# Performance work log

Measured on AMD Instinct MI355X. Metric: run time of the kernel, lower is better.

The kernel has to match this reference:

```python
import jax, jax.numpy as jnp
from jax import lax
import numpy as np

D = 1024   # d_model
N = 64     # d_state
P = 64     # headdim
H = 16     # nheads = d_inner // headdim (d_inner = d_model)
E = 8      # n_experts
R = 8      # LoRA rank
OM = 32    # omega_dim
MEMD = 384 # memory vector dim
KC = 4     # d_conv
Bz, Lz = 2, 1024


def setup_inputs() -> dict:
    key = jax.random.key(0)
    it = iter(jax.random.split(key, 48))
    def nrm(shape, s=0.02):
        return jax.random.normal(next(it), shape, jnp.float32) * s
    return dict(
        x=jax.random.normal(next(it), (Bz, Lz, D), jnp.float32),
        wkv_state=nrm((Bz, N, N), 0.1),
        x_prev=jax.random.normal(next(it), (Bz, 1, D), jnp.float32),
        memory_vec=jax.random.normal(next(it), (Bz, MEMD), jnp.float32),
        rag_state=nrm((Bz, N, N), 0.1),
        ssd_state=nrm((Bz, H, P, N), 0.1),
        conv_state=nrm((Bz, D, KC), 0.1),
        norm_scale=jnp.ones((D,), jnp.float32), norm_bias=jnp.zeros((D,), jnp.float32),
        W_in=nrm((2 * D, D)), conv_w=nrm((D, KC), 0.1), conv_b=jnp.zeros((D,), jnp.float32),
        W_dt=nrm((H, D)), dt_bias=jnp.full((H,), -2.0, jnp.float32),
        A_log=jnp.log(jnp.linspace(0.5, 8.0, H)).astype(jnp.float32),
        W_B=nrm((N, D)), W_C=nrm((N, D)), W_ssd_out=nrm((D, D)),
        W_r=nrm((N, D)), W_k=nrm((N, D)), W_v=nrm((N, D)), W_w=nrm((N, D)),
        W_rwkv_out=nrm((D, N)),
        W_skew=nrm((OM, OM), 0.1), W_om_in=nrm((OM, D)), W_om_out=nrm((D, OM)),
        W_router=nrm((E, D)), lora_A=nrm((E, D, R)), lora_B=nrm((E, R, D)),
        W_nov=nrm((1, 2 * D)), b_nov=jnp.zeros((1,), jnp.float32),
        W_ragq=nrm((N, D)), W_rago=nrm((D, N)),
        W_mq=nrm((MEMD, D)), W_mp=nrm((D, MEMD)),
        W_mg=nrm((1, D + MEMD)), b_mg=jnp.zeros((1,), jnp.float32),
    )


def _layernorm(x, s, b):
    m = x.mean(-1, keepdims=True)
    v = ((x - m) ** 2).mean(-1, keepdims=True)
    return (x - m) * lax.rsqrt(v + 1e-5) * s + b


def _forward(x, wkv_state, x_prev, memory_vec, rag_state, ssd_state, conv_state,
             norm_scale, norm_bias, W_in, conv_w, conv_b, W_dt, dt_bias, A_log,
             W_B, W_C, W_ssd_out, W_r, W_k, W_v, W_w, W_rwkv_out,
             W_skew, W_om_in, W_om_out, W_router, lora_A, lora_B, W_nov, b_nov,
             W_ragq, W_rago, W_mq, W_mp, W_mg, b_mg):
    Bb, Ll, _ = x.shape
    residual = x
    xn = _layernorm(x, norm_scale, norm_bias)
    # ---- TarsCoreBlock: Mamba-2 SSD scan + RWKV-7 wkv scan + gated fusion ----
    zu = xn @ W_in.T
    z, u = zu[..., :D], zu[..., D:]
    # depthwise causal conv1d with rolling conv_state [B, D, KC]
    u_cat = jnp.concatenate([conv_state.transpose(0, 2, 1), u], axis=1)  # [B, KC+L, D]
    acc = conv_b
    for k in range(KC):
        acc = acc + u_cat[:, k:k + Ll, :] * conv_w[:, k]
    uc = jax.nn.silu(acc)
    conv_new = u_cat[:, Ll:, :].transpose(0, 2, 1)
    dt = jax.nn.softplus(xn @ W_dt.T + dt_bias)   # [B,L,H]
    A = -jnp.exp(A_log)                            # [H], negative decay rates
    Bm = xn @ W_B.T                                # [B,L,N]
    Cm = xn @ W_C.T                                # [B,L,N]
    uh = uc.reshape(Bb, Ll, H, P)
    def ssd_step(h, inp):
        dt_t, u_t, b_t, c_t = inp                  # [B,H],[B,H,P],[B,N],[B,N]
        h = h * jnp.exp(dt_t * A)[..., None, None] + (dt_t[..., None, None] * u_t[..., None]) * b_t[:, None, None, :]
        return h, jnp.einsum('bhpn,bn->bhp', h, c_t)
    ssd_new, ys = lax.scan(ssd_step, ssd_state,
                           (dt.transpose(1, 0, 2), uh.transpose(1, 0, 2, 3),
                            Bm.transpose(1, 0, 2), Cm.transpose(1, 0, 2)))
    y_ssd = ys.transpose(1, 0, 2, 3).reshape(Bb, Ll, D) @ W_ssd_out.T
    # RWKV-7 style wkv recurrence with time-shift mixing
    x_shift = jnp.concatenate([x_prev, xn[:, :-1]], axis=1)
    mix = 0.5 * (xn + x_shift)
    r, kk, v = mix @ W_r.T, mix @ W_k.T, mix @ W_v.T
    w = jnp.exp(-jnp.exp(mix @ W_w.T))             # per-channel decay in (0,1)
    def rwkv_step(S, inp):
        r_t, k_t, v_t, w_t = inp
        S = S * w_t[:, :, None] + v_t[:, :, None] * k_t[:, None, :]
        return S, jnp.einsum('bij,bj->bi', S, r_t)
    wkv_new, yr = lax.scan(rwkv_step, wkv_state,
                           (r.transpose(1, 0, 2), kk.transpose(1, 0, 2),
                            v.transpose(1, 0, 2), w.transpose(1, 0, 2)))
    y_rwkv = yr.transpose(1, 0, 2) @ W_rwkv_out.T
    core_out = jax.nn.silu(z) * y_ssd + y_rwkv     # WuNeng fusion
    x1 = residual + core_out
    x_prev_new = xn[:, -1:, :]
    # ---- RAG injection from compressed rag_state ----
    q = x1.mean(1) @ W_ragq.T                      # [B,N]
    info = jnp.einsum('bij,bj->bi', rag_state, q)
    x1 = x1 + 0.1 * (info @ W_rago.T)[:, None, :]
    # ---- Omega-SSM: Cayley SO(n) rotation in omega subspace ----
    Ask = 0.5 * (W_skew - W_skew.T)
    I = jnp.eye(OM, dtype=x.dtype)
    Qc = jnp.linalg.solve(I - Ask, I + Ask)        # orthogonal via Cayley map
    x1 = x1 + ((x1 @ W_om_in.T) @ Qc.T) @ W_om_out.T
    # ---- MoLE: sparse top-2 low-rank (LoRA) experts ----
    probs = jax.nn.softmax(x1 @ W_router.T, axis=-1)  # [B,L,E]
    _, topi = lax.top_k(probs, 2)
    mask = jax.nn.one_hot(topi, E, dtype=x.dtype).sum(-2)
    gate = probs * mask
    gate = gate / (gate.sum(-1, keepdims=True) + 1e-9)
    down = jnp.einsum('bld,edr->bler', x1, lora_A)    # [B,L,E,R]
    x2 = x1 + jnp.einsum('bler,erd->bld', down * gate[..., None], lora_B)
    aux = E * jnp.sum(probs.mean((0, 1)) * mask.mean((0, 1)))
    # ---- NoveltyGate blended residual ----
    h_old, h_new = residual.mean(1), x2.mean(1)
    novelty = jax.nn.sigmoid(jnp.concatenate([h_old, h_new], -1) @ W_nov.T + b_nov)[:, 0]
    n = novelty[:, None, None]
    x3 = n * x2 + (1.0 - n) * residual
    # ---- Cosine-gated memory fusion ----
    h_post = x3.mean(1)
    hq = h_post @ W_mq.T
    sim = (hq * memory_vec).sum(-1) / (jnp.linalg.norm(hq, axis=-1) * jnp.linalg.norm(memory_vec, axis=-1) + 1e-8)
    gm = jax.nn.sigmoid(jnp.concatenate([h_post, memory_vec], -1) @ W_mg.T + b_mg)[:, 0]
    x4 = x3 + (sim * gm)[:, None, None] * (memory_vec @ W_mp.T)[:, None, :]
    return x4, wkv_new, x_prev_new, ssd_new, conv_new, aux


def reference(x, wkv_state, x_prev, memory_vec, rag_state, ssd_state, conv_state,
              norm_scale, norm_bias, W_in, conv_w, conv_b, W_dt, dt_bias, A_log,
              W_B, W_C, W_ssd_out, W_r, W_k, W_v, W_w, W_rwkv_out,
              W_skew, W_om_in, W_om_out, W_router, lora_A, lora_B, W_nov, b_nov,
              W_ragq, W_rago, W_mq, W_mp, W_mg, b_mg):
    return _forward(x, wkv_state, x_prev, memory_vec, rag_state, ssd_state, conv_state,
                    norm_scale, norm_bias, W_in, conv_w, conv_b, W_dt, dt_bias, A_log,
                    W_B, W_C, W_ssd_out, W_r, W_k, W_v, W_w, W_rwkv_out,
                    W_skew, W_om_in, W_om_out, W_router, lora_A, lora_B, W_nov, b_nov,
                    W_ragq, W_rago, W_mq, W_mp, W_mg, b_mg)
```

## Files before the change

kernel.cpp:

```cpp
#include <hip/hip_runtime.h>
#include <hip/hip_bf16.h>

#define DD    1024
#define NN    64
#define HH    16
#define EE    8
#define OMM   32
#define MEMDD 384
#define BB    2
#define LL    1024
#define TT    2048

#define OFF_X4    0
#define OFF_WKV   2097152
#define OFF_XPREV 2105344
#define OFF_SSD   2107392
#define OFF_CONV  2238464
#define OFF_AUX   2246656

typedef unsigned short u16;
typedef __attribute__((ext_vector_type(8))) short short8;
typedef __attribute__((ext_vector_type(4))) float f32x4;

__device__ __forceinline__ float us2f(u16 u){ return __uint_as_float(((unsigned)u)<<16); }
// ... 217 lines not shown
        for (int n=0;n<4;++n) acc[m][n] = (f32x4){0.f,0.f,0.f,0.f};
    for (int k0=0; k0<K; k0+=64){
        #pragma unroll
        for (int i=0;i<2;++i){
            int row = wid*16 + i*8 + lr;
            gl_lds16(Ag + (size_t)row*K + k0 + lc8, &Asm[(wid*16 + i*8)*64]);
        }
        #pragma unroll
        for (int i=0;i<4;++i){
            int row = wid*32 + i*8 + lr;
            gl_lds16(Wg + (size_t)row*K + k0 + lc8, &Bsm[(wid*32 + i*8)*64]);
        }
        __syncthreads();
        #pragma unroll
        for (int ks=0; ks<2; ++ks){
            short8 af[2], bf[4];
            #pragma unroll
            for (int m=0;m<2;++m)
                af[m] = *(const short8*)&Asm[(wr*32 + m*16 + l15)*64 + ks*32 + quad*8];
            #pragma unroll
            for (int n=0;n<4;++n)
                bf[n] = *(const short8*)&Bsm[(wc*64 + n*16 + l15)*64 + ks*32 + quad*8];
            #pragma unroll
            for (int m=0;m<2;++m)
                #pragma unroll
                for (int n=0;n<4;++n)
                    acc[m][n] = __builtin_amdgcn_mfma_f32_16x16x32_bf16(af[m], bf[n], acc[m][n], 0,0,0);
        }
        __syncthreads();
    }
    int ns1 = N - Nsplit;
    #pragma unroll
    for (int m=0;m<2;++m){
        #pragma unroll
        for (int n=0;n<4;++n){
            int col = bn + wc*64 + n*16 + l15;
            #pragma unroll
            for (int i=0;i<4;++i){
                int row = bm + wr*32 + m*16 + quad*4 + i;
                float v = acc[m][n][i];
                if (col < Nsplit){
                    size_t id = (size_t)row*Nsplit + col;
                    if (c0bf) ((u16*)C0)[id] = f2us(v);
                    else C0[id] = (addto ? C0[id] : 0.f) + v;
                } else {
                    size_t id = (size_t)row*ns1 + (col - Nsplit);
                    C1[id] = v;
                }
            }
        }
    }
}

__global__ __launch_bounds__(256)
void gemm_big_k(const u16* __restrict__ A, const u16* __restrict__ W,
                float* __restrict__ C0, float* __restrict__ C1,
                int N, int K, int Nsplit, int addto){
    __shared__ u16 Asm[64*64];
    __shared__ u16 Bsm[128*64];
    gemm_body(Asm, Bsm, A, W, C0, C1, N, K, Nsplit, addto, 0, blockIdx.x, blockIdx.y);
}

__global__ __launch_bounds__(256)
void gemm_big2_k(const u16* __restrict__ A, const u16* __restrict__ W,
                 float* __restrict__ C0, float* __restrict__ C1,
                 int N, int K, int Nsplit){
    __shared__ u16 Asm[128*64];
    __shared__ u16 Bsm[128*64];
    int tid = threadIdx.x;
    int wid = tid >> 6, lane = tid & 63;
    int l15 = lane & 15, quad = lane >> 4;
    int wr = wid >> 1, wc = wid & 1;
    int bm = blockIdx.x*128, bn = blockIdx.y*128;
    int lr = lane >> 3;
    int lc8 = (lane & 7)*8;
    const u16* Ag = A + (size_t)bm*K;
    const u16* Wg = W + (size_t)bn*K;
    f32x4 acc[4][4];
    #pragma unroll
    for (int m=0;m<4;++m)
        #pragma unroll
        for (int n=0;n<4;++n) acc[m][n] = (f32x4){0.f,0.f,0.f,0.f};
    for (int k0=0; k0<K; k0+=64){
        #pragma unroll
        for (int i=0;i<4;++i){
            int row = wid*32 + i*8 + lr;
            gl_lds16(Ag + (size_t)row*K + k0 + lc8, &Asm[(wid*32 + i*8)*64]);
        }
        #pragma unroll
        for (int i=0;i<4;++i){
            int row = wid*32 + i*8 + lr;
            gl_lds16(Wg + (size_t)row*K + k0 + lc8, &Bsm[(wid*32 + i*8)*64]);
        }
        __syncthreads();
        #pragma unroll
        for (int ks=0; ks<2; ++ks){
            short8 af[4], bf[4];
            #pragma unroll
            for (int m=0;m<4;++m)
                af[m] = *(const short8*)&Asm[(wr*64 + m*16 + l15)*64 + ks*32 + quad*8];
            #pragma unroll
            for (int n=0;n<4;++n)
                bf[n] = *(const short8*)&Bsm[(wc*64 + n*16 + l15)*64 + ks*32 + quad*8];
            #pragma unroll
            for (int m=0;m<4;++m)
                #pragma unroll
                for (int n=0;n<4;++n)
                    acc[m][n] = __builtin_amdgcn_mfma_f32_16x16x32_bf16(af[m], bf[n], acc[m][n], 0,0,0);
        }
        __syncthreads();
    }
    int ns1 = N - Nsplit;
    #pragma unroll
    for (int m=0;m<4;++m){
        #pragma unroll
        for (int n=0;n<4;++n){
            int col = bn + wc*64 + n*16 + l15;
            #pragma unroll
            for (int i=0;i<4;++i){
                int row = bm + wr*64 + m*16 + quad*4 + i;
                float v = acc[m][n][i];
                if (col < Nsplit){
                    C0[(size_t)row*Nsplit + col] = v;
                } else {
                    C1[(size_t)row*ns1 + (col - Nsplit)] = v;
                }
            }
        }
    }
}

__global__ __launch_bounds__(256)
void proj_dual_k(const u16* __restrict__ xnbf, const u16* __restrict__ wcatxn,
                 float* __restrict__ pcat2_as_f, float* __restrict__ dtraw,
                 const u16* __restrict__ mixbf, const u16* __restrict__ wcatmix,
                 float* __restrict__ rkvw){
    __shared__ u16 Asm[64*64];
    __shared__ u16 Bsm[128*64];
    if (blockIdx.y < 2)
        gemm_body(Asm, Bsm, xnbf, wcatxn, pcat2_as_f, dtraw, 256, 1024, 128, 0, 1, blockIdx.x, blockIdx.y);
    else
        gemm_body(Asm, Bsm, mixbf, wcatmix, rkvw, dtraw, 256, 1024, 256, 0, 0, blockIdx.x, blockIdx.y-2);
}

__global__ __launch_bounds__(256)
void out_dual_k(const u16* __restrict__ ysbf, const u16* __restrict__ wbfss, float* __restrict__ s1,
                const u16* __restrict__ ybf, const u16* __restrict__ wbfrw, float* __restrict__ s2){
    __shared__ u16 Asm[64*64];
    __shared__ u16 Bsm[128*64];
    if (blockIdx.y < 8)
        gemm_body(Asm, Bsm, ysbf, wbfss, s1, (float*)nullptr, 1024, 1024, 1024, 0, 0, blockIdx.x, blockIdx.y);
    else
        gemm_body(Asm, Bsm, ybf, wbfrw, s2, (float*)nullptr, 1024, 64, 1024, 0, 0, blockIdx.x, blockIdx.y-8);
}

__global__ __launch_bounds__(256)
void cmx_k(const float* __restrict__ u, const float* __restrict__ xn,
           const void* __restrict__ cs, const void* __restrict__ cw, const void* __restrict__ cb,
           const void* __restrict__ xprev,
           float* __restrict__ uc, u16* __restrict__ mixbf, void* __restrict__ out,
           const int* modep){
    const int m = *modep;
    int idx = blockIdx.x*256 + threadIdx.x;
    int t = idx >> 10, d = idx & 1023;
    int b = t >> 10, l = t & 1023;
    float acc = LD(cb, d, m);
    #pragma unroll
    for (int k=0;k<4;++k){
        int i = l + k;
        float xv = (i < 4) ? LD(cs, ((size_t)(b*DD + d))*4 + i, m)
                           : u[(size_t)(t + k - 4)*DD + d];
        acc += xv * LD(cw, d*4 + k, m);
    }
    uc[idx] = acc * sigf(acc);
    float xc = xn[idx];
    float xp = (l == 0) ? LD(xprev, (size_t)b*DD + d, m) : xn[idx - DD];
    mixbf[idx] = f2us(0.5f*(xc + xp));
    if (l >= LL-4)
        ST(out, OFF_CONV + (size_t)b*DD*4 + d*4 + (l - (LL-4)), u[idx], m);
}

#define LDSS 72
__global__ __launch_bounds__(256)
void ssdA_k(const u16* __restrict__ pcat2, const float* __restrict__ dtraw,
            const float* __restrict__ uc,
            const void* __restrict__ A_log, const void* __restrict__ dt_bias,
            float* __restrict__ ys, float* __restrict__ Scb, float* __restrict__ cumsb,
            const int* modep){
    __shared__ u16 Bs[64*LDSS];
    __shared__ u16 Cs[64*LDSS];
    __shared__ u16 BTw[64*LDSS];
    __shared__ u16 XTs[64*LDSS];
    __shared__ float cums[64];
    __shared__ float dts_raw[64];
    const int m = *modep;
    int tid = threadIdx.x;
    int wid = tid >> 6, lane = tid & 63;
    int blk = blockIdx.x;
    int b = blk >> 8, h = (blk >> 4) & 15, c = blk & 15;
    int l16 = lane & 15, quad = lane >> 4;
    int r = tid >> 2;
    int cb4 = (tid & 3) * 16;
    float Ah = -expf(LD(A_log, h, m));
    int t0 = c*64;
    const u16* Pg = pcat2 + (size_t)(b*LL + t0)*128;
    #pragma unroll
// ... 43 lines not shown
    __syncthreads();
    f32x4 gacc[4];
    #pragma unroll
    for (int nt=0;nt<4;++nt) gacc[nt]=(f32x4){0.f,0.f,0.f,0.f};
    #pragma unroll
    for (int ks=0; ks<64; ks+=32){
        short8 af = *(const short8*)&Cs[(wid*16 + l16)*LDSS + ks + quad*8];
        #pragma unroll
        for (int nt=0;nt<4;++nt){
            short8 bf = *(const short8*)&Bs[(nt*16 + l16)*LDSS + ks + quad*8];
            gacc[nt] = __builtin_amdgcn_mfma_f32_16x16x32_bf16(af, bf, gacc[nt], 0,0,0);
        }
    }
    __syncthreads();
    #pragma unroll
    for (int nt=0;nt<4;++nt){
        int s_loc = nt*16 + l16;
        #pragma unroll
        for (int i=0;i<4;++i){
            int t_loc = wid*16 + quad*4 + i;
            float gv = (s_loc <= t_loc) ? gacc[nt][i]*expf(cums[t_loc]-cums[s_loc]) : 0.f;
            Bs[t_loc*LDSS + s_loc] = f2us(gv);
        }
    }
    __syncthreads();
    f32x4 acc2[4], acc4[4];
    #pragma unroll
    for (int nt=0;nt<4;++nt){ acc2[nt]=(f32x4){0.f,0.f,0.f,0.f}; acc4[nt]=(f32x4){0.f,0.f,0.f,0.f}; }
    #pragma unroll
    for (int ks=0; ks<64; ks+=32){
        short8 sf = *(const short8*)&Bs[(wid*16 + l16)*LDSS + ks + quad*8];
        short8 xf = *(const short8*)&XTs[(wid*16 + l16)*LDSS + ks + quad*8];
        #pragma unroll
        for (int nt=0;nt<4;++nt){
            short8 xo = *(const short8*)&XTs[(nt*16 + l16)*LDSS + ks + quad*8];
            acc2[nt] = __builtin_amdgcn_mfma_f32_16x16x32_bf16(sf, xo, acc2[nt], 0,0,0);
            short8 bo = *(const short8*)&BTw[(nt*16 + l16)*LDSS + ks + quad*8];
            acc4[nt] = __builtin_amdgcn_mfma_f32_16x16x32_bf16(xf, bo, acc4[nt], 0,0,0);
        }
    }
    #pragma unroll
    for (int nt=0;nt<4;++nt){
        int col = nt*16 + l16;
        #pragma unroll
        for (int i=0;i<4;++i){
            int row = wid*16 + quad*4 + i;
            ys[(size_t)(b*LL + t0 + row)*DD + h*64 + col] = acc2[nt][i];
            Scb[(size_t)blk*4096 + row*64 + col] = acc4[nt][i];
        }
    }
}

#define FS 68
__global__ __launch_bounds__(256)
void rwkvA_k(const float* __restrict__ rkvw,
             float* __restrict__ yr, float* __restrict__ Slb, float* __restrict__ Wcumb){
    __shared__ float wch[64*FS], vch[64*FS], kch[64*FS], rch[64*FS];
    __shared__ float Wc[64*FS];
    __shared__ float part[4*8*64];
    int tid = threadIdx.x;
    int wid = tid >> 6, lane = tid & 63;
    int blk = blockIdx.x;
    int b = blk >> 4, c = blk & 15;
    int t0 = c*64;
    int r = tid >> 2, c4 = (tid & 3)*16;
    const float* base = rkvw + (size_t)(b*LL + t0)*256;
    #pragma unroll
    for (int i=0;i<4;++i){
        int cc = c4 + i*4;
        *(float4*)&rch[r*FS+cc] = *(const float4*)(base + (size_t)r*256 + cc);
        *(float4*)&kch[r*FS+cc] = *(const float4*)(base + (size_t)r*256 + 64 + cc);
        *(float4*)&vch[r*FS+cc] = *(const float4*)(base + (size_t)r*256 + 128 + cc);
        float4 wv = *(const float4*)(base + (size_t)r*256 + 192 + cc);
        wch[r*FS+cc+0] = expf(-expf(wv.x));
        wch[r*FS+cc+1] = expf(-expf(wv.y));
        wch[r*FS+cc+2] = expf(-expf(wv.z));
        wch[r*FS+cc+3] = expf(-expf(wv.w));
    }
    __syncthreads();
    if (wid == 0){
        float cum = 1.f;
        for (int t=0;t<64;++t){ cum *= wch[t*FS+lane]; Wc[t*FS+lane] = cum; }
    }
    __syncthreads();
    #pragma unroll
    for (int q=0;q<16;++q){
        int idx = q*256 + tid;
        int t = idx >> 6, i = idx & 63;
        Wcumb[(size_t)blk*4096 + idx] = Wc[t*FS + i];
    }
    float S[16];
    #pragma unroll
    for (int jj=0;jj<16;++jj) S[jj]=0.f;
    int jb = wid*16;
    for (int t8=0; t8<8; ++t8){
        float ya[8];
        #pragma unroll
        for (int u=0;u<8;++u){
            int t = t8*8+u;
            float wv = wch[t*FS+lane];
            float vv = vch[t*FS+lane];
            float yy0=0.f, yy1=0.f, yy2=0.f, yy3=0.f;
            #pragma unroll
            for (int jj=0;jj<16;jj+=4){
                float k0v = kch[t*FS + jb + jj+0], r0v = rch[t*FS + jb + jj+0];
                float k1v = kch[t*FS + jb + jj+1], r1v = rch[t*FS + jb + jj+1];
                float k2v = kch[t*FS + jb + jj+2], r2v = rch[t*FS + jb + jj+2];
                float k3v = kch[t*FS + jb + jj+3], r3v = rch[t*FS + jb + jj+3];
                S[jj+0] = S[jj+0]*wv + vv*k0v; yy0 += S[jj+0]*r0v;
                S[jj+1] = S[jj+1]*wv + vv*k1v; yy1 += S[jj+1]*r1v;
                S[jj+2] = S[jj+2]*wv + vv*k2v; yy2 += S[jj+2]*r2v;
                S[jj+3] = S[jj+3]*wv + vv*k3v; yy3 += S[jj+3]*r3v;
            }
            ya[u] = (yy0+yy1)+(yy2+yy3);
        }
        #pragma unroll
        for (int u=0;u<8;++u) part[wid*512 + u*64 + lane] = ya[u];
        __syncthreads();
        #pragma unroll
        for (int it=0; it<2; ++it){
            int e = it*256 + tid;
            int u = e >> 6, i = e & 63;
            float y = part[0*512 + u*64 + i] + part[1*512 + u*64 + i]
                    + part[2*512 + u*64 + i] + part[3*512 + u*64 + i];
            yr[(size_t)(b*LL + t0 + t8*8 + u)*NN + i] = y;
        }
        __syncthreads();
    }
    #pragma unroll
    for (int jj=0;jj<16;++jj)
        Slb[(size_t)blk*4096 + (size_t)lane*64 + jb + jj] = S[jj];
}

__global__ __launch_bounds__(256)
void sb_k(const void* __restrict__ ssd_state, const float* __restrict__ Scb,
          const float* __restrict__ cumsb, u16* __restrict__ hinb,
          const void* __restrict__ wkv_state, const float* __restrict__ Slb,
          const float* __restrict__ Wcumb, u16* __restrict__ hinr,
          void* __restrict__ out, const int* modep){
    const int m = *modep;
    int tid = threadIdx.x;
    if (blockIdx.x < 32){
        int bh = blockIdx.x;
        float h[16];
        #pragma unroll
        for (int i=0;i<16;++i)
            h[i] = LD(ssd_state, (size_t)bh*4096 + i*256 + tid, m);
        for (int c=0; c<16; ++c){
            int blk = bh*16 + c;
            float efull = expf(cumsb[(size_t)blk*64 + 63]);
            #pragma unroll
            for (int i=0;i<16;++i){
                hinb[(size_t)blk*4096 + i*256 + tid] = f2us(h[i]);
                h[i] = efull*h[i] + Scb[(size_t)blk*4096 + i*256 + tid];
            }
        }
        #pragma unroll
        for (int i=0;i<16;++i)
            ST(out, OFF_SSD + (size_t)bh*4096 + i*256 + tid, h[i], m);
    } else {
        int b = blockIdx.x - 32;
        float S[16];
        #pragma unroll
        for (int q=0;q<16;++q)
            S[q] = LD(wkv_state, (size_t)b*4096 + q*256 + tid, m);
        for (int c=0;c<16;++c){
            int blk = b*16+c;
            #pragma unroll
            for (int q=0;q<16;++q){
                int idx = q*256+tid;
                int i = idx >> 6;
                hinr[(size_t)blk*4096 + idx] = f2us(S[q]);
                float P = Wcumb[(size_t)blk*4096 + 63*64 + i];
                S[q] = S[q]*P + Slb[(size_t)blk*4096 + idx];
            }
        }
        #pragma unroll
        for (int q=0;q<16;++q)
            ST(out, OFF_WKV + (size_t)b*4096 + q*256 + tid, S[q], m);
    }
}

__global__ __launch_bounds__(256)
// ... 45 lines not shown
                float e = expf(cumsb[(size_t)blk*64 + row]);
                size_t id = (size_t)(b*LL + t0 + row)*DD + h*64 + col;
                ysbf[id] = f2us(ys[id] + e*acc[nt][i]);
            }
        }
    } else {
        int blk = blockIdx.x - 512;
        int b = blk >> 4, c = blk & 15;
        int t0 = c*64;
        const float* Rg = rkvw + (size_t)(b*LL + t0)*256;
        #pragma unroll
        for (int i=0;i<4;++i){
            int cc = cb4 + i*4;
            float4 g = *(const float4*)(Rg + (size_t)r*256 + cc);
            u16* d2 = &T0[r*LDSS + cc];
            d2[0]=f2us(g.x); d2[1]=f2us(g.y); d2[2]=f2us(g.z); d2[3]=f2us(g.w);
            ushort4 hv = *(const ushort4*)(hinr + (size_t)blk*4096 + r*64 + cc);
            u16* hd = &T1[r*LDSS + cc];
            hd[0]=hv.x; hd[1]=hv.y; hd[2]=hv.z; hd[3]=hv.w;
        }
        __syncthreads();
        f32x4 acc[4];
        #pragma unroll
        for (int nt=0;nt<4;++nt) acc[nt]=(f32x4){0.f,0.f,0.f,0.f};
        #pragma unroll
        for (int ks=0; ks<64; ks+=32){
            short8 af = *(const short8*)&T0[(wid*16 + l16)*LDSS + ks + quad*8];
            #pragma unroll
            for (int nt=0;nt<4;++nt){
                short8 hf = *(const short8*)&T1[(nt*16 + l16)*LDSS + ks + quad*8];
                acc[nt] = __builtin_amdgcn_mfma_f32_16x16x32_bf16(af, hf, acc[nt], 0,0,0);
            }
        }
        #pragma unroll
        for (int nt=0;nt<4;++nt){
            int col = nt*16 + l16;
            #pragma unroll
            for (int i=0;i<4;++i){
                int row = wid*16 + quad*4 + i;
                float Wt = Wcumb[(size_t)blk*4096 + row*64 + col];
                size_t id = (size_t)(b*LL + t0 + row)*NN + col;
                ybf[id] = f2us(yr[id] + Wt*acc[nt][i]);
            }
        }
    }
}

__global__ __launch_bounds__(256)
void fuse_mean_k(const float* __restrict__ z, const float* __restrict__ s1,
                 const float* __restrict__ s2, const void* __restrict__ xin,
                 float* __restrict__ x1, float* __restrict__ mean1, const int* modep){
    const int m = *modep;
    int bid = blockIdx.x;
    int lc = bid & 15, dc = (bid >> 4) & 3, b = bid >> 6;
    int d = dc*256 + threadIdx.x;
    float sum = 0.f;
    int l0 = lc*64;
    for (int l=l0; l<l0+64; ++l){
        size_t idx = (size_t)(b*LL + l)*DD + d;
        float zl = z[idx];
        float v = LD(xin, idx, m) + zl*sigf(zl)*s1[idx] + s2[idx];
        x1[idx] = v;
        sum += v;
    }
    atomicAdd(&mean1[b*DD + d], sum*(1.f/LL));
}

__global__ __launch_bounds__(256)
void ragA_k(const float* __restrict__ mean1, const void* __restrict__ W_ragq,
            float* __restrict__ qb, const int* modep){
    const int m = *modep;
    int bx = blockIdx.x;
    int b = bx >> 4;
    int tid = threadIdx.x, wid = tid >> 6, lane = tid & 63;
    int row = (bx & 15)*4 + wid;
    float s = 0.f;
    size_t wo = (size_t)row*DD;
    #pragma unroll
    for (int it=0; it<16; ++it)
        s += LD(W_ragq, wo + it*64 + lane, m) * mean1[(b<<10) + it*64 + lane];
    s = wave_sum64(s);
    if (lane == 0) qb[b*64 + row] = s;
}

__global__ __launch_bounds__(256)
void ragB_k(const float* __restrict__ qb, const void* __restrict__ rag_state,
            float* __restrict__ infob, const int* modep){
    const int m = *modep;
    int bx = blockIdx.x;
    int b = bx >> 4;
    int tid = threadIdx.x, wid = tid >> 6, lane = tid & 63;
    int row = (bx & 15)*4 + wid;
    float s = LD(rag_state, (size_t)(b*64+row)*64 + lane, m) * qb[b*64 + lane];
    s = wave_sum64(s);
    if (lane == 0) infob[b*64 + row] = s;
}

__global__ __launch_bounds__(256)
void ragC_k(const float* __restrict__ infob, const void* __restrict__ W_rago,
            float* __restrict__ ragd, const int* modep){
    const int m = *modep;
    int bx = blockIdx.x;
    int b = bx >> 6;
    int tid = threadIdx.x, wid = tid >> 6, lane = tid & 63;
    int r0 = (bx & 63)*16 + wid*4;
    float iv = infob[b*64 + lane];
    #pragma unroll
    for (int rr=0; rr<4; ++rr){
        int d = r0 + rr;
        float s = iv * LD(W_rago, (size_t)d*64 + lane, m);
        s = wave_sum64(s);
        if (lane == 0) ragd[(b<<10) + d] = 0.1f*s;
    }
}

__global__ __launch_bounds__(256)
void addrag_k(float* __restrict__ x1, const float* __restrict__ ragd, u16* __restrict__ xbf){
    int i4 = (blockIdx.x*256 + threadIdx.x)*4;
    int b = i4 >> 20, d = i4 & 1023;
    #pragma unroll
    for (int j=0;j<4;++j){
        float v = x1[i4+j] + ragd[(b<<10) + d + j];
        x1[i4+j] = v;
        xbf[i4+j] = f2us(v);
    }
}

__global__ __launch_bounds__(256)
void moe_k(const float* __restrict__ x1, const void* __restrict__ W_router,
           const void* __restrict__ lora_A, const void* __restrict__ lora_B,
           float* __restrict__ x2, float* __restrict__ probs8, int* __restrict__ eidx,
           const int* modep){
    const int m = *modep;
    int t = blockIdx.x, tid = threadIdx.x;
    int wid = tid >> 6, lane = tid & 63;
    __shared__ float xs[1024];
    __shared__ float red[32];
    __shared__ float logits[8];
    __shared__ float downs[16];
    __shared__ float gsh[2];
    __shared__ int esh[2];
    #pragma unroll
    for (int i=0;i<4;i++) xs[i*256+tid] = x1[(size_t)t*DD + i*256+tid];
    __syncthreads();
    {
        float p0=0.f, p1=0.f;
        size_t w0o = (size_t)(2*wid)*DD, w1o = (size_t)(2*wid+1)*DD;
        #pragma unroll
        for (int it=0; it<16; ++it){
            float xv = xs[it*64 + lane];
            p0 += xv * LD(W_router, w0o + it*64 + lane, m);
            p1 += xv * LD(W_router, w1o + it*64 + lane, m);
        }
        p0 = wave_sum64(p0); p1 = wave_sum64(p1);
        if (lane == 0){ logits[2*wid] = p0; logits[2*wid+1] = p1; }
    }
    __syncthreads();
    if (tid == 0){
        float mx = logits[0];
// ... 3 lines not shown
        for (int e2=0;e2<8;++e2) pe[e2] /= sum;
        int e0=0; for (int e2=1;e2<8;++e2) if (pe[e2]>pe[e0]) e0=e2;
        int e1=(e0==0)?1:0; for (int e2=0;e2<8;++e2) if (e2!=e0 && pe[e2]>pe[e1]) e1=e2;
        float gs = pe[e0]+pe[e1]+1e-9f;
        gsh[0]=pe[e0]/gs; gsh[1]=pe[e1]/gs; esh[0]=e0; esh[1]=e1;
        #pragma unroll
        for (int e2=0;e2<8;++e2) probs8[(size_t)t*8 + e2] = pe[e2];
        eidx[t*2+0]=e0; eidx[t*2+1]=e1;
    }
    __syncthreads();
    {
        int ei = wid & 1, half = wid >> 1;
        int e2 = esh[ei];
        int dsub = lane >> 3;
        size_t ao = (size_t)e2*8192 + (size_t)half*4096;
        float acc = 0.f;
        #pragma unroll
        for (int c=0; c<64; ++c){
            float xv = xs[half*512 + c*8 + dsub];
            acc += xv * LD(lora_A, ao + c*64 + lane, m);
        }
        acc += __shfl_xor(acc, 8);
        acc += __shfl_xor(acc, 16);
        acc += __shfl_xor(acc, 32);
        if (lane < 8) red[wid*8 + lane] = acc;
    }
    __syncthreads();
    if (tid < 16){
        int ei = tid >> 3, r = tid & 7;
        downs[ei*8 + r] = red[ei*8 + r] + red[(ei+2)*8 + r];
    }
    __syncthreads();
    {
        int e0=esh[0], e1=esh[1]; float g0=gsh[0], g1=gsh[1];
        #pragma unroll
        for (int i=0;i<4;i++){
            int d = i*256+tid;
            float acc=0.f;
            size_t b0 = (size_t)e0*8192 + d;
            size_t b1 = (size_t)e1*8192 + d;
            #pragma unroll
            for (int r=0;r<8;++r) acc += g0*downs[r]*LD(lora_B, b0 + (size_t)r*1024, m)
                                       + g1*downs[8+r]*LD(lora_B, b1 + (size_t)r*1024, m);
            x2[(size_t)t*DD + d] = xs[d] + acc;
        }
    }
}

__global__ __launch_bounds__(256)
void colmean2_k(const float* __restrict__ x2, const void* __restrict__ xin,
                float* __restrict__ hnew, float* __restrict__ hold, const int* modep){
    const int m = *modep;
    int bid = blockIdx.x;
    int lc = bid & 15, dc = (bid >> 4) & 3, b = bid >> 6;
    int d = dc*256 + threadIdx.x;
    float s = 0.f;
    int l0 = lc*64;
    if (blockIdx.y == 0){
        for (int l=l0; l<l0+64; ++l) s += x2[(size_t)(b*LL + l)*DD + d];
        atomicAdd(&hnew[b*DD + d], s*(1.f/LL));
    } else {
        for (int l=l0; l<l0+64; ++l) s += LD(xin, (size_t)(b*LL + l)*DD + d, m);
        atomicAdd(&hold[b*DD + d], s*(1.f/LL));
    }
}

__global__ __launch_bounds__(256)
void hq2_k(const float* __restrict__ hold, const float* __restrict__ hnew,
           const void* __restrict__ W_nov, const void* __restrict__ b_nov,
           const void* __restrict__ W_mq, float* __restrict__ hqb, const int* modep){
    const int m = *modep;
    int b = blockIdx.x, tid = threadIdx.x;
    int wid = tid >> 6, lane = tid & 63;
    int r0 = blockIdx.y*16;
    __shared__ float hs[1024];
    __shared__ float red[256];
    float p=0.f;
    #pragma unroll
    for (int i=0;i<4;i++){ int d=i*256+tid;
        p += hold[b*DD+d]*LD(W_nov,d,m) + hnew[b*DD+d]*LD(W_nov,DD+d,m); }
    float n = sigf(block_sum256(p, red) + LD(b_nov,0,m));
    #pragma unroll
    for (int i=0;i<4;i++){ int d=i*256+tid;
        hs[d] = n*hnew[b*DD+d] + (1.f-n)*hold[b*DD+d]; }
    __syncthreads();
    #pragma unroll
    for (int rr=0; rr<4; ++rr){
        int row = r0 + wid*4 + rr;
        float s = 0.f;
        size_t wo = (size_t)row*DD;
        #pragma unroll
        for (int it=0; it<16; ++it) s += LD(W_mq, wo + it*64 + lane, m) * hs[it*64 + lane];
        s = wave_sum64(s);
        if (lane == 0) hqb[b*MEMDD + row] = s;
    }
}

__global__ __launch_bounds__(256)
void gate2_k(const float* __restrict__ hold, const float* __restrict__ hnew,
             const void* __restrict__ W_nov, const void* __restrict__ b_nov,
             const float* __restrict__ hqb, const void* __restrict__ memv,
             const void* __restrict__ W_mg, const void* __restrict__ b_mg,
             const float* __restrict__ probs8, const int* __restrict__ eidx,
             float* __restrict__ scal, void* __restrict__ out, const int* modep){
    const int m = *modep;
    int b = blockIdx.x, tid = threadIdx.x;
    int wid = tid >> 6, lane = tid & 63;
    __shared__ float red[256];
    __shared__ float rps[4][8];
    __shared__ float rcs[4][8];
    float p=0.f;
    #pragma unroll
    for (int i=0;i<4;i++){ int d=i*256+tid;
        p += hold[b*DD+d]*LD(W_nov,d,m) + hnew[b*DD+d]*LD(W_nov,DD+d,m); }
    float n = sigf(block_sum256(p, red) + LD(b_nov,0,m));
// ... 72 lines not shown
    cb rag_state = d_in[4];
    cb ssd_state = d_in[5];
    cb conv_state= d_in[6];
    cb nscale    = d_in[7];
    cb nbias     = d_in[8];
    cb W_in      = d_in[9];
    cb conv_w    = d_in[10];
    cb conv_b    = d_in[11];
    cb W_dt      = d_in[12];
    cb dt_bias   = d_in[13];
    cb A_log     = d_in[14];
    cb W_B       = d_in[15];
    cb W_C       = d_in[16];
    cb W_ssd_out = d_in[17];
    cb W_r       = d_in[18];
    cb W_k       = d_in[19];
    cb W_v       = d_in[20];
    cb W_w       = d_in[21];
    cb W_rwkv_out= d_in[22];
    cb W_skew    = d_in[23];
    cb W_om_in   = d_in[24];
    cb W_om_out  = d_in[25];
    cb W_router  = d_in[26];
    cb lora_A    = d_in[27];
    cb lora_B    = d_in[28];
    cb W_nov     = d_in[29];
    cb b_nov     = d_in[30];
    cb W_ragq    = d_in[31];
    cb W_rago    = d_in[32];
    cb W_mq      = d_in[33];
    cb W_mp      = d_in[34];
    cb W_mg      = d_in[35];
    cb b_mg      = d_in[36];

    float* ws = (float*)d_ws;
    size_t o = 0;
    float* xn_x1   = ws + o; o += (size_t)TT*DD;
    float* z_x2    = ws + o; o += (size_t)TT*DD;
    float* u_ys    = ws + o; o += (size_t)TT*DD;
    float* ucb     = ws + o; o += (size_t)TT*DD;
    float* s2b     = ws + o; o += (size_t)TT*DD;
    float* dtraw   = ws + o; o += (size_t)TT*128;
    float* rkvw    = ws + o; o += (size_t)TT*256;
    float* yrb     = ws + o; o += (size_t)TT*NN;
    float* Qcb     = ws + o; o += 1024;
    float* Scb     = ws + o; o += (size_t)512*4096;
    float* cumsb   = ws + o; o += (size_t)512*64;
    float* Wcumb   = ws + o; o += (size_t)32*4096;
    float* Slb     = ws + o; o += (size_t)32*4096;
    u16*   hinb    = (u16*)(ws + o); o += (size_t)512*4096/2;
    u16*   hinr    = (u16*)(ws + o); o += (size_t)32*4096/2;
    float* mean1   = ws + o; o += BB*DD;
    float* ragd    = ws + o; o += BB*DD;
    float* qb      = ws + o; o += BB*NN;
    float* infob   = ws + o; o += BB*NN;
    float* holdb   = ws + o; o += BB*DD;
    float* hnewb   = ws + o; o += BB*DD;
    float* scal    = ws + o; o += 16;
    float* mdel    = ws + o; o += BB*DD;
    float* hqb     = ws + o; o += BB*MEMDD;
    float* probs8  = ws + o; o += (size_t)TT*8;
    int*   eidx    = (int*)(ws + o); o += (size_t)TT*2;
    int*   flag    = (int*)(ws + o); o += 16;
    u16*   xnbf    = (u16*)(ws + o); o += (size_t)TT*DD/2;
    u16*   mixbf   = (u16*)(ws + o); o += (size_t)TT*DD/2;
    u16*   x1bf    = (u16*)(ws + o); o += (size_t)TT*DD/2;
    u16*   ysbf    = (u16*)(ws + o); o += (size_t)TT*DD/2;
    u16*   ybf     = (u16*)(ws + o); o += (size_t)TT*NN/2;
    u16*   pcat2   = (u16*)(ws + o); o += (size_t)TT*128/2;
    u16*   wbfin   = (u16*)(ws + o); o += (size_t)2*DD*DD/2;
    u16*   wbfss   = (u16*)(ws + o); o += (size_t)DD*DD/2;
    u16*   wbfrw   = (u16*)(ws + o); o += (size_t)DD*NN/2;
    u16*   wcatxn  = (u16*)(ws + o); o += (size_t)256*DD/2;
    u16*   wcatmix = (u16*)(ws + o); o += (size_t)256*DD/2;
    u16*   wcombbf = (u16*)(ws + o); o += (size_t)DD*DD/2;

    dim3 blk(256);

    hipLaunchKernelGGL(prep_k, dim3(1024,8), blk, 0, stream,
                       nscale, flag, mean1, holdb, hnewb,
                       W_in, wbfin, W_ssd_out, wbfss, W_rwkv_out, wbfrw,
                       W_B, W_C, W_dt, wcatxn, W_r, W_k, W_v, W_w, wcatmix,
                       memv, W_mp, mdel, W_skew, Qcb);
    hipLaunchKernelGGL(ln_k, dim3(TT + 1024), blk, 0, stream, x, nscale, nbias, xn_x1, xnbf, d_out,
                       W_om_out, Qcb, W_om_in, wcombbf, flag);
    hipLaunchKernelGGL(gemm_big2_k, dim3(TT/128, 16), blk, 0, stream, xnbf, wbfin,
                       z_x2, u_ys, 2*DD, DD, DD);
    hipLaunchKernelGGL(cmx_k, dim3(TT*DD/256), blk, 0, stream, u_ys, xn_x1,
                       conv_state, conv_w, conv_b, x_prev, ucb, mixbf, d_out, flag);
    hipLaunchKernelGGL(proj_dual_k, dim3(TT/64, 4), blk, 0, stream,
                       xnbf, wcatxn, (float*)pcat2, dtraw, mixbf, wcatmix, rkvw);
    hipLaunchKernelGGL(ssdA_k, dim3(512), blk, 0, stream, pcat2, dtraw, ucb, A_log, dt_bias,
                       u_ys , Scb, cumsb, flag);
    hipLaunchKernelGGL(rwkvA_k, dim3(32), blk, 0, stream, rkvw, yrb, Slb, Wcumb);
    hipLaunchKernelGGL(sb_k, dim3(34), blk, 0, stream, ssd_state, Scb, cumsb, hinb,
                       wkv_state, Slb, Wcumb, hinr, d_out, flag);
    hipLaunchKernelGGL(sc_k, dim3(544), blk, 0, stream, pcat2, hinb, cumsb, u_ys, ysbf,
                       rkvw, hinr, Wcumb, yrb, ybf);
    hipLaunchKernelGGL(out_dual_k, dim3(TT/64, 16), blk, 0, stream,
                       ysbf, wbfss, ucb , ybf, wbfrw, s2b);
    hipLaunchKernelGGL(fuse_mean_k, dim3(128), blk, 0, stream, z_x2, ucb, s2b, x,
                       xn_x1 , mean1, flag);
    hipLaunchKernelGGL(ragA_k, dim3(32), blk, 0, stream, mean1, W_ragq, qb, flag);
    hipLaunchKernelGGL(ragB_k, dim3(32), blk, 0, stream, qb, rag_state, infob, flag);
    hipLaunchKernelGGL(ragC_k, dim3(128), blk, 0, stream, infob, W_rago, ragd, flag);
    hipLaunchKernelGGL(addrag_k, dim3(TT*DD/1024), blk, 0, stream, xn_x1, ragd, x1bf);
    hipLaunchKernelGGL(gemm_big_k, dim3(TT/64, 8), blk, 0, stream, x1bf, wcombbf,
                       xn_x1, (float*)nullptr, DD, DD, DD, 1);
    hipLaunchKernelGGL(moe_k, dim3(TT), blk, 0, stream, xn_x1, W_router, lora_A, lora_B, z_x2,
                       probs8, eidx, flag);
    hipLaunchKernelGGL(colmean2_k, dim3(128,2), blk, 0, stream, z_x2, x, hnewb, holdb, flag);
    hipLaunchKernelGGL(hq2_k, dim3(BB,24), blk, 0, stream, holdb, hnewb, W_nov, b_nov,
                       W_mq, hqb, flag);
    hipLaunchKernelGGL(gate2_k, dim3(BB), blk, 0, stream, holdb, hnewb, W_nov, b_nov,
                       hqb, memv, W_mg, b_mg, probs8, eidx, scal, d_out, flag);
    hipLaunchKernelGGL(final_k, dim3(TT*DD/1024), blk, 0, stream, z_x2, x, scal, mdel, d_out, flag);
}
```

Baseline: 461.5 us.

## Use 128x128 GEMM tiles broadly, fuse RAG kernels, widen rwkvA and mean reductions

Generalizes the 128x128-tile GEMM body (with bf16 output and accumulate options) and uses it for the projection, output, and combined-weight GEMMs instead of the 64x128 tile. The three tiny RAG kernels become one kernel that keeps intermediates in shared memory. rwkvA now runs 512 threads per block, and the column-mean reductions use 4x more blocks with shorter loops. Together these target launch overhead, data reuse in the GEMMs, and low parallelism in the small kernels. The cost is fewer GEMM blocks (less parallelism) and redundant RAG q/info computation in every block.

```diff
diff --git a/kernel.cpp b/kernel.cpp
--- a/kernel.cpp
+++ b/kernel.cpp
@@ -293,26 +293,15 @@
     }
 }
 
-__global__ __launch_bounds__(256)
-void gemm_big_k(const u16* __restrict__ A, const u16* __restrict__ W,
+__device__ __forceinline__ void gemm2_body(u16* Asm, u16* Bsm,
+                const u16* __restrict__ A, const u16* __restrict__ W,
                 float* __restrict__ C0, float* __restrict__ C1,
-                int N, int K, int Nsplit, int addto){
-    __shared__ u16 Asm[64*64];
-    __shared__ u16 Bsm[128*64];
-    gemm_body(Asm, Bsm, A, W, C0, C1, N, K, Nsplit, addto, 0, blockIdx.x, blockIdx.y);
-}
-
-__global__ __launch_bounds__(256)
-void gemm_big2_k(const u16* __restrict__ A, const u16* __restrict__ W,
-                 float* __restrict__ C0, float* __restrict__ C1,
-                 int N, int K, int Nsplit){
-    __shared__ u16 Asm[128*64];
-    __shared__ u16 Bsm[128*64];
+                int N, int K, int Nsplit, int addto, int c0bf, int bx, int by){
     int tid = threadIdx.x;
     int wid = tid >> 6, lane = tid & 63;
     int l15 = lane & 15, quad = lane >> 4;
     int wr = wid >> 1, wc = wid & 1;
-    int bm = blockIdx.x*128, bn = blockIdx.y*128;
+    int bm = bx*128, bn = by*128;
     int lr = lane >> 3;
     int lc8 = (lane & 7)*8;
     const u16* Ag = A + (size_t)bm*K;
@@ -362,13 +351,25 @@
                 int row = bm + wr*64 + m*16 + quad*4 + i;
                 float v = acc[m][n][i];
                 if (col < Nsplit){
-                    C0[(size_t)row*Nsplit + col] = v;
+                    size_t id = (size_t)row*Nsplit + col;
+                    if (c0bf) ((u16*)C0)[id] = f2us(v);
+                    else C0[id] = (addto ? C0[id] : 0.f) + v;
                 } else {
-                    C1[(size_t)row*ns1 + (col - Nsplit)] = v;
+                    size_t id = (size_t)row*ns1 + (col - Nsplit);
+                    C1[id] = v;
                 }
             }
         }
     }
+}
+
+__global__ __launch_bounds__(256)
+void gemm2_k(const u16* __restrict__ A, const u16* __restrict__ W,
+             float* __restrict__ C0, float* __restrict__ C1,
+             int N, int K, int Nsplit, int addto, int c0bf){
+    __shared__ u16 Asm[128*64];
+    __shared__ u16 Bsm[128*64];
+    gemm2_body(Asm, Bsm, A, W, C0, C1, N, K, Nsplit, addto, c0bf, blockIdx.x, blockIdx.y);
 }
 
 __global__ __launch_bounds__(256)
@@ -376,23 +377,25 @@
                  float* __restrict__ pcat2_as_f, float* __restrict__ dtraw,
                  const u16* __restrict__ mixbf, const u16* __restrict__ wcatmix,
                  float* __restrict__ rkvw){
-    __shared__ u16 Asm[64*64];
+    __shared__ u16 Asm[128*64];
     __shared__ u16 Bsm[128*64];
     if (blockIdx.y < 2)
-        gemm_body(Asm, Bsm, xnbf, wcatxn, pcat2_as_f, dtraw, 256, 1024, 128, 0, 1, blockIdx.x, blockIdx.y);
+        gemm2_body(Asm, Bsm, xnbf, wcatxn, pcat2_as_f, dtraw, 256, 1024, 128, 0, 1, blockIdx.x, blockIdx.y);
     else
-        gemm_body(Asm, Bsm, mixbf, wcatmix, rkvw, dtraw, 256, 1024, 256, 0, 0, blockIdx.x, blockIdx.y-2);
+        gemm2_body(Asm, Bsm, mixbf, wcatmix, rkvw, (float*)nullptr, 256, 1024, 256, 0, 0, blockIdx.x, blockIdx.y-2);
 }
 
 __global__ __launch_bounds__(256)
 void out_dual_k(const u16* __restrict__ ysbf, const u16* __restrict__ wbfss, float* __restrict__ s1,
                 const u16* __restrict__ ybf, const u16* __restrict__ wbfrw, float* __restrict__ s2){
-    __shared__ u16 Asm[64*64];
+    __shared__ u16 Asm[128*64];
     __shared__ u16 Bsm[128*64];
-    if (blockIdx.y < 8)
-        gemm_body(Asm, Bsm, ysbf, wbfss, s1, (float*)nullptr, 1024, 1024, 1024, 0, 0, blockIdx.x, blockIdx.y);
-    else
+    if (blockIdx.y < 8){
+        if (blockIdx.x >= 16) return;
+        gemm2_body(Asm, Bsm, ysbf, wbfss, s1, (float*)nullptr, 1024, 1024, 1024, 0, 0, blockIdx.x, blockIdx.y);
+    } else {
         gemm_body(Asm, Bsm, ybf, wbfrw, s2, (float*)nullptr, 1024, 64, 1024, 0, 0, blockIdx.x, blockIdx.y-8);
+    }
 }
 
 __global__ __launch_bounds__(256)
@@ -542,22 +545,22 @@
 }
 
 #define FS 68
-__global__ __launch_bounds__(256)
+__global__ __launch_bounds__(512)
 void rwkvA_k(const float* __restrict__ rkvw,
              float* __restrict__ yr, float* __restrict__ Slb, float* __restrict__ Wcumb){
     __shared__ float wch[64*FS], vch[64*FS], kch[64*FS], rch[64*FS];
     __shared__ float Wc[64*FS];
-    __shared__ float part[4*8*64];
+    __shared__ float part[8*512];
     int tid = threadIdx.x;
     int wid = tid >> 6, lane = tid & 63;
     int blk = blockIdx.x;
     int b = blk >> 4, c = blk & 15;
     int t0 = c*64;
-    int r = tid >> 2, c4 = (tid & 3)*16;
+    int r = tid >> 3, c8 = (tid & 7)*8;
     const float* base = rkvw + (size_t)(b*LL + t0)*256;
     #pragma unroll
-    for (int i=0;i<4;++i){
-        int cc = c4 + i*4;
+    for (int i=0;i<2;++i){
+        int cc = c8 + i*4;
         *(float4*)&rch[r*FS+cc] = *(const float4*)(base + (size_t)r*256 + cc);
         *(float4*)&kch[r*FS+cc] = *(const float4*)(base + (size_t)r*256 + 64 + cc);
         *(float4*)&vch[r*FS+cc] = *(const float4*)(base + (size_t)r*256 + 128 + cc);
@@ -574,15 +577,15 @@
     }
     __syncthreads();
     #pragma unroll
-    for (int q=0;q<16;++q){
-        int idx = q*256 + tid;
+    for (int q=0;q<8;++q){
+        int idx = q*512 + tid;
         int t = idx >> 6, i = idx & 63;
         Wcumb[(size_t)blk*4096 + idx] = Wc[t*FS + i];
     }
-    float S[16];
-    #pragma unroll
-    for (int jj=0;jj<16;++jj) S[jj]=0.f;
-    int jb = wid*16;
+    float S[8];
+    #pragma unroll
+    for (int jj=0;jj<8;++jj) S[jj]=0.f;
+    int jb = wid*8;
     for (int t8=0; t8<8; ++t8){
         float ya[8];
         #pragma unroll
@@ -590,35 +593,30 @@
             int t = t8*8+u;
             float wv = wch[t*FS+lane];
             float vv = vch[t*FS+lane];
-            float yy0=0.f, yy1=0.f, yy2=0.f, yy3=0.f;
-            #pragma unroll
-            for (int jj=0;jj<16;jj+=4){
+            float yy0=0.f, yy1=0.f;
+            #pragma unroll
+            for (int jj=0;jj<8;jj+=2){
                 float k0v = kch[t*FS + jb + jj+0], r0v = rch[t*FS + jb + jj+0];
                 float k1v = kch[t*FS + jb + jj+1], r1v = rch[t*FS + jb + jj+1];
-                float k2v = kch[t*FS + jb + jj+2], r2v = rch[t*FS + jb + jj+2];
-                float k3v = kch[t*FS + jb + jj+3], r3v = rch[t*FS + jb + jj+3];
                 S[jj+0] = S[jj+0]*wv + vv*k0v; yy0 += S[jj+0]*r0v;
                 S[jj+1] = S[jj+1]*wv + vv*k1v; yy1 += S[jj+1]*r1v;
-                S[jj+2] = S[jj+2]*wv + vv*k2v; yy2 += S[jj+2]*r2v;
-                S[jj+3] = S[jj+3]*wv + vv*k3v; yy3 += S[jj+3]*r3v;
             }
-            ya[u] = (yy0+yy1)+(yy2+yy3);
+            ya[u] = yy0+yy1;
         }
         #pragma unroll
         for (int u=0;u<8;++u) part[wid*512 + u*64 + lane] = ya[u];
         __syncthreads();
-        #pragma unroll
-        for (int it=0; it<2; ++it){
-            int e = it*256 + tid;
-            int u = e >> 6, i = e & 63;
-            float y = part[0*512 + u*64 + i] + part[1*512 + u*64 + i]
-                    + part[2*512 + u*64 + i] + part[3*512 + u*64 + i];
+        {
+            int u = tid >> 6, i = tid & 63;
+            float y = 0.f;
+            #pragma unroll
+            for (int w=0;w<8;++w) y += part[w*512 + u*64 + i];
             yr[(size_t)(b*LL + t0 + t8*8 + u)*NN + i] = y;
         }
         __syncthreads();
     }
     #pragma unroll
-    for (int jj=0;jj<16;++jj)
+    for (int jj=0;jj<8;++jj)
         Slb[(size_t)blk*4096 + (size_t)lane*64 + jb + jj] = S[jj];
 }
 
@@ -770,11 +768,11 @@
                  float* __restrict__ x1, float* __restrict__ mean1, const int* modep){
     const int m = *modep;
     int bid = blockIdx.x;
-    int lc = bid & 15, dc = (bid >> 4) & 3, b = bid >> 6;
+    int lc = bid & 63, dc = (bid >> 6) & 3, b = bid >> 8;
     int d = dc*256 + threadIdx.x;
     float sum = 0.f;
-    int l0 = lc*64;
-    for (int l=l0; l<l0+64; ++l){
+    int l0 = lc*16;
+    for (int l=l0; l<l0+16; ++l){
         size_t idx = (size_t)(b*LL + l)*DD + d;
         float zl = z[idx];
         float v = LD(xin, idx, m) + zl*sigf(zl)*s1[idx] + s2[idx];
@@ -785,44 +783,40 @@
 }
 
 __global__ __launch_bounds__(256)
-void ragA_k(const float* __restrict__ mean1, const void* __restrict__ W_ragq,
-            float* __restrict__ qb, const int* modep){
-    const int m = *modep;
-    int bx = blockIdx.x;
-    int b = bx >> 4;
-    int tid = threadIdx.x, wid = tid >> 6, lane = tid & 63;
-    int row = (bx & 15)*4 + wid;
-    float s = 0.f;
-    size_t wo = (size_t)row*DD;
-    #pragma unroll
-    for (int it=0; it<16; ++it)
-        s += LD(W_ragq, wo + it*64 + lane, m) * mean1[(b<<10) + it*64 + lane];
-    s = wave_sum64(s);
-    if (lane == 0) qb[b*64 + row] = s;
-}
-
-__global__ __launch_bounds__(256)
-void ragB_k(const float* __restrict__ qb, const void* __restrict__ rag_state,
-            float* __restrict__ infob, const int* modep){
-    const int m = *modep;
-    int bx = blockIdx.x;
-    int b = bx >> 4;
-    int tid = threadIdx.x, wid = tid >> 6, lane = tid & 63;
-    int row = (bx & 15)*4 + wid;
-    float s = LD(rag_state, (size_t)(b*64+row)*64 + lane, m) * qb[b*64 + lane];
-    s = wave_sum64(s);
-    if (lane == 0) infob[b*64 + row] = s;
-}
-
-__global__ __launch_bounds__(256)
-void ragC_k(const float* __restrict__ infob, const void* __restrict__ W_rago,
+void rag2_k(const float* __restrict__ mean1, const void* __restrict__ W_ragq,
+            const void* __restrict__ rag_state, const void* __restrict__ W_rago,
             float* __restrict__ ragd, const int* modep){
     const int m = *modep;
     int bx = blockIdx.x;
     int b = bx >> 6;
     int tid = threadIdx.x, wid = tid >> 6, lane = tid & 63;
+    __shared__ float ms[1024];
+    __shared__ float q[64];
+    __shared__ float info[64];
+    #pragma unroll
+    for (int i=0;i<4;i++) ms[i*256+tid] = mean1[(b<<10) + i*256 + tid];
+    __syncthreads();
+    #pragma unroll
+    for (int rr=0; rr<16; ++rr){
+        int row = wid*16 + rr;
+        float s = 0.f;
+        size_t wo = (size_t)row*DD;
+        #pragma unroll
+        for (int it=0; it<16; ++it) s += LD(W_ragq, wo + it*64 + lane, m) * ms[it*64 + lane];
+        s = wave_sum64(s);
+        if (lane == 0) q[row] = s;
+    }
+    __syncthreads();
+    #pragma unroll
+    for (int rr=0; rr<16; ++rr){
+        int row = wid*16 + rr;
+        float s = LD(rag_state, (size_t)(b*64+row)*64 + lane, m) * q[lane];
+        s = wave_sum64(s);
+        if (lane == 0) info[row] = s;
+    }
+    __syncthreads();
     int r0 = (bx & 63)*16 + wid*4;
-    float iv = infob[b*64 + lane];
+    float iv = info[lane];
     #pragma unroll
     for (int rr=0; rr<4; ++rr){
         int d = r0 + rr;
@@ -932,15 +926,15 @@
                 float* __restrict__ hnew, float* __restrict__ hold, const int* modep){
     const int m = *modep;
     int bid = blockIdx.x;
-    int lc = bid & 15, dc = (bid >> 4) & 3, b = bid >> 6;
+    int lc = bid & 63, dc = (bid >> 6) & 3, b = bid >> 8;
     int d = dc*256 + threadIdx.x;
     float s = 0.f;
-    int l0 = lc*64;
+    int l0 = lc*16;
     if (blockIdx.y == 0){
-        for (int l=l0; l<l0+64; ++l) s += x2[(size_t)(b*LL + l)*DD + d];
+        for (int l=l0; l<l0+16; ++l) s += x2[(size_t)(b*LL + l)*DD + d];
         atomicAdd(&hnew[b*DD + d], s*(1.f/LL));
     } else {
-        for (int l=l0; l<l0+64; ++l) s += LD(xin, (size_t)(b*LL + l)*DD + d, m);
+        for (int l=l0; l<l0+16; ++l) s += LD(xin, (size_t)(b*LL + l)*DD + d, m);
         atomicAdd(&hold[b*DD + d], s*(1.f/LL));
     }
 }
@@ -1119,8 +1113,6 @@
     u16*   hinr    = (u16*)(ws + o); o += (size_t)32*4096/2;
     float* mean1   = ws + o; o += BB*DD;
     float* ragd    = ws + o; o += BB*DD;
-    float* qb      = ws + o; o += BB*NN;
-    float* infob   = ws + o; o += BB*NN;
     float* holdb   = ws + o; o += BB*DD;
     float* hnewb   = ws + o; o += BB*DD;
     float* scal    = ws + o; o += 16;
@@ -1151,32 +1143,31 @@
                        memv, W_mp, mdel, W_skew, Qcb);
     hipLaunchKernelGGL(ln_k, dim3(TT + 1024), blk, 0, stream, x, nscale, nbias, xn_x1, xnbf, d_out,
                        W_om_out, Qcb, W_om_in, wcombbf, flag);
-    hipLaunchKernelGGL(gemm_big2_k, dim3(TT/128, 16), blk, 0, stream, xnbf, wbfin,
-                       z_x2, u_ys, 2*DD, DD, DD);
+    hipLaunchKernelGGL(gemm2_k, dim3(TT/128, 16), blk, 0, stream, xnbf, wbfin,
+                       z_x2, u_ys, 2*DD, DD, DD, 0, 0);
     hipLaunchKernelGGL(cmx_k, dim3(TT*DD/256), blk, 0, stream, u_ys, xn_x1,
                        conv_state, conv_w, conv_b, x_prev, ucb, mixbf, d_out, flag);
-    hipLaunchKernelGGL(proj_dual_k, dim3(TT/64, 4), blk, 0, stream,
+    hipLaunchKernelGGL(proj_dual_k, dim3(TT/128, 4), blk, 0, stream,
                        xnbf, wcatxn, (float*)pcat2, dtraw, mixbf, wcatmix, rkvw);
     hipLaunchKernelGGL(ssdA_k, dim3(512), blk, 0, stream, pcat2, dtraw, ucb, A_log, dt_bias,
                        u_ys , Scb, cumsb, flag);
-    hipLaunchKernelGGL(rwkvA_k, dim3(32), blk, 0, stream, rkvw, yrb, Slb, Wcumb);
+    hipLaunchKernelGGL(rwkvA_k, dim3(32), dim3(512), 0, stream, rkvw, yrb, Slb, Wcumb);
     hipLaunchKernelGGL(sb_k, dim3(34), blk, 0, stream, ssd_state, Scb, cumsb, hinb,
                        wkv_state, Slb, Wcumb, hinr, d_out, flag);
     hipLaunchKernelGGL(sc_k, dim3(544), blk, 0, stream, pcat2, hinb, cumsb, u_ys, ysbf,
                        rkvw, hinr, Wcumb, yrb, ybf);
     hipLaunchKernelGGL(out_dual_k, dim3(TT/64, 16), blk, 0, stream,
                        ysbf, wbfss, ucb , ybf, wbfrw, s2b);
-    hipLaunchKernelGGL(fuse_mean_k, dim3(128), blk, 0, stream, z_x2, ucb, s2b, x,
+    hipLaunchKernelGGL(fuse_mean_k, dim3(512), blk, 0, stream, z_x2, ucb, s2b, x,
                        xn_x1 , mean1, flag);
-    hipLaunchKernelGGL(ragA_k, dim3(32), blk, 0, stream, mean1, W_ragq, qb, flag);
-    hipLaunchKernelGGL(ragB_k, dim3(32), blk, 0, stream, qb, rag_state, infob, flag);
-    hipLaunchKernelGGL(ragC_k, dim3(128), blk, 0, stream, infob, W_rago, ragd, flag);
+    hipLaunchKernelGGL(rag2_k, dim3(128), blk, 0, stream, mean1, W_ragq, rag_state, W_rago,
+                       ragd, flag);
     hipLaunchKernelGGL(addrag_k, dim3(TT*DD/1024), blk, 0, stream, xn_x1, ragd, x1bf);
-    hipLaunchKernelGGL(gemm_big_k, dim3(TT/64, 8), blk, 0, stream, x1bf, wcombbf,
-                       xn_x1, (float*)nullptr, DD, DD, DD, 1);
+    hipLaunchKernelGGL(gemm2_k, dim3(TT/128, 8), blk, 0, stream, x1bf, wcombbf,
+                       xn_x1, (float*)nullptr, DD, DD, DD, 1, 0);
     hipLaunchKernelGGL(moe_k, dim3(TT), blk, 0, stream, xn_x1, W_router, lora_A, lora_B, z_x2,
                        probs8, eidx, flag);
-    hipLaunchKernelGGL(colmean2_k, dim3(128,2), blk, 0, stream, z_x2, x, hnewb, holdb, flag);
+    hipLaunchKernelGGL(colmean2_k, dim3(512,2), blk, 0, stream, z_x2, x, hnewb, holdb, flag);
     hipLaunchKernelGGL(hq2_k, dim3(BB,24), blk, 0, stream, holdb, hnewb, W_nov, b_nov,
                        W_mq, hqb, flag);
     hipLaunchKernelGGL(gate2_k, dim3(BB), blk, 0, stream, holdb, hnewb, W_nov, b_nov,
```

Measured after the change: 482.5 us. 1.05x slower.
